# Optimization experiments

Hardware: AMD Instinct MI355X
Metric: run time of the kernel (lower is better)

Reference implementation:

```python
import jax, jax.numpy as jnp
import numpy as np

N = 50000   # num nodes
E = 800000  # num edges (avg degree 16)
D = 64      # input feature dim
H = 64      # hidden dim
O = 32      # output dim


def setup_inputs() -> dict:
    key = jax.random.key(0)
    ks = jax.random.split(key, 8)
    def lin(k, fan_in, fan_out):
        # Kaiming-uniform-ish init, stored as [in, out] so forward is x @ W
        bound = 1.0 / np.sqrt(fan_in)
        return jax.random.uniform(k, (fan_in, fan_out), jnp.float32, -bound, bound)
    return {
        "x": jax.random.normal(ks[0], (N, D), jnp.float32),
        "edge_index": jax.random.randint(ks[1], (2, E), 0, N),
        "W_in1": lin(ks[2], D, H),
        "W_neigh1": lin(ks[3], D, H),
        "bias1": jnp.zeros((H,), jnp.float32),
        "W_in2": lin(ks[4], H, H),
        "W_neigh2": lin(ks[5], H, H),
        "bias2": jnp.zeros((H,), jnp.float32),
        "W_out": lin(ks[6], H, O),
        "b_out": jnp.zeros((O,), jnp.float32),
    }


def reference(x, edge_index, W_in1, W_neigh1, bias1, W_in2, W_neigh2, bias2, W_out, b_out):
    row, col = edge_index[0], edge_index[1]  # source, target
    # get_laplacian(sym) + remove_self_loops + negate -> norm = d^-1/2[row] * d^-1/2[col]
    deg = jax.ops.segment_sum(jnp.ones((E,), x.dtype), row, num_segments=N)
    dinv = jnp.where(deg > 0, deg ** -0.5, jnp.zeros((), x.dtype))
    norm = dinv[row] * dinv[col]  # [E]

    def conv(h, W_in, W_neigh, bias):
        # message: gather transformed source features, scale by per-edge norm
        msg = (h @ W_neigh)[row] * norm[:, None]          # [E, out]
        agg = jax.ops.segment_sum(msg, col, num_segments=N)  # scatter-add -> [N, out]
        return h @ W_in + agg + bias[None, :]

    h = jax.nn.relu(conv(x, W_in1, W_neigh1, bias1))
    h = jax.nn.relu(conv(h, W_in2, W_neigh2, bias2))
    return h @ W_out + b_out[None, :]  # variant='equi': per-node output [N, O]
```

## Files before the change

### kernel.cpp

```cpp
#include <hip/hip_runtime.h>
#include <hip/hip_bf16.h>


#define NCHUNK 32
#define NRANGE_B 8
#define HIST_B2 6272
#define SMEM1 100352

typedef __attribute__((ext_vector_type(8))) short bfrag;
typedef __attribute__((ext_vector_type(4))) float f32x4;

template <bool RELU, bool PRESCALE>
__device__ __forceinline__ void gemm_tile16(
    const float* h, const float* __restrict__ dinv,
    const short* Wn_f, const short* Wi_f, const float* b_s,
    __hip_bfloat16* __restrict__ t, float* agg, int r0, int lane, int N) {
  const int m = lane & 15;
  const int quad = lane >> 4;

  bfrag Bn[4][2], Bi[4][2];
#pragma unroll
  for (int ct = 0; ct < 4; ++ct)
#pragma unroll
    for (int kb = 0; kb < 2; ++kb) {
      Bn[ct][kb] = *(const bfrag*)&Wn_f[((ct * 2 + kb) * 64 + lane) * 8];
      Bi[ct][kb] = *(const bfrag*)&Wi_f[((ct * 2 + kb) * 64 + lane) * 8];
    }

  const int arow = r0 + m;
  bfrag A[2];
#pragma unroll
  for (int kb = 0; kb < 2; ++kb) {
    bfrag av = {};
    if (arow < N) {
      const float* src = &h[(size_t)arow * 64 + kb * 32 + quad * 8];
      float4 f0 = *(const float4*)src;
      float4 f1 = *(const float4*)(src + 4);
      float tmp[8] = {f0.x, f0.y, f0.z, f0.w, f1.x, f1.y, f1.z, f1.w};
#pragma unroll
      for (int j = 0; j < 8; ++j) {
        float v = RELU ? fmaxf(tmp[j], 0.f) : tmp[j];
        __hip_bfloat16 hb = __float2bfloat16(v);
        av[j] = *(short*)&hb;
      }
    }
    A[kb] = av;
  }

  f32x4 accT[4], accA[4];
#pragma unroll
  for (int ct = 0; ct < 4; ++ct) {
    f32x4 z = {0.f, 0.f, 0.f, 0.f};
    accT[ct] = z;
    accA[ct] = z;
  }
#pragma unroll
  for (int ct = 0; ct < 4; ++ct) {
    accT[ct] = __builtin_amdgcn_mfma_f32_16x16x32_bf16(A[0], Bn[ct][0], accT[ct], 0, 0, 0);
    accT[ct] = __builtin_amdgcn_mfma_f32_16x16x32_bf16(A[1], Bn[ct][1], accT[ct], 0, 0, 0);
    accA[ct] = __builtin_amdgcn_mfma_f32_16x16x32_bf16(A[0], Bi[ct][0], accA[ct], 0, 0, 0);
    accA[ct] = __builtin_amdgcn_mfma_f32_16x16x32_bf16(A[1], Bi[ct][1], accA[ct], 0, 0, 0);
  }

#pragma unroll
  for (int reg = 0; reg < 4; ++reg) {
    int r = r0 + quad * 4 + reg;
    if (r < N) {
      float dv = PRESCALE ? dinv[r] : 1.0f;
#pragma unroll
      for (int ct = 0; ct < 4; ++ct) {
        int col = ct * 16 + m;
        float tv = PRESCALE ? accT[ct][reg] * dv : accT[ct][reg];
        t[(size_t)r * 64 + col] = __float2bfloat16(tv);
        agg[(size_t)r * 64 + col] = accA[ct][reg] + b_s[col];
      }
    }
  }
}

__device__ __forceinline__ void stage_W_frag(const float* __restrict__ Wn,
                                             const float* __restrict__ Wi,
                                             short* Wn_f, short* Wi_f,
                                             int tid, int nthr) {
  for (int i = tid; i < 4096; i += nthr) {
    int k = i >> 6, n = i & 63;
    int dst = (((n >> 4) * 2 + (k >> 5)) * 64 + ((k >> 3) & 3) * 16 + (n & 15)) * 8 + (k & 7);
    __hip_bfloat16 a = __float2bfloat16(Wn[i]);
    __hip_bfloat16 b = __float2bfloat16(Wi[i]);
    Wn_f[dst] = *(short*)&a;
    Wi_f[dst] = *(short*)&b;
  }
}

__global__ __launch_bounds__(1024) void k_hist_gemm1(
    const int* __restrict__ ei, unsigned short* __restrict__ partial,
    const float* __restrict__ x,
    const float* __restrict__ Wn, const float* __restrict__ Wi,
    const float* __restrict__ bias,
    __hip_bfloat16* __restrict__ t, float* __restrict__ agg,
    int N, int E, int gemmBlocks) {
  __shared__ __align__(16) char smem[SMEM1];
  const int tid = threadIdx.x;

  if ((int)blockIdx.x < gemmBlocks) {
    short* Wn_f = (short*)smem;
    short* Wi_f = (short*)(smem + 8192);
    float* b_s = (float*)(smem + 16384);
    stage_W_frag(Wn, Wi, Wn_f, Wi_f, tid, 1024);
    if (tid < 64) b_s[tid] = bias[tid];
    __syncthreads();
    int w = tid >> 6;
    int lane = tid & 63;
    int r0 = blockIdx.x * 256 + w * 16;
    gemm_tile16<false, false>(x, nullptr, Wn_f, Wi_f, b_s, t, agg, r0, lane, N);
    return;
  }

  int* histw = (int*)smem;
  int bid = blockIdx.x - gemmBlocks;
  int c = bid % NCHUNK;
  int a = bid / NCHUNK;
  const int* ids = ei + (size_t)a * E;
  const int sw = (N + 1) & ~1;
  const int words = sw >> 1;
  for (int i = tid; i < words; i += 1024) histw[i] = 0;
  __syncthreads();
  int e0 = (int)((long long)E * c / NCHUNK);
  int e1 = (int)((long long)E * (c + 1) / NCHUNK);
  for (int e = e0 + tid; e < e1; e += 1024) {
    int s = ids[e];
    atomicAdd(&histw[s >> 1], 1 << ((s & 1) * 16));
  }
  __syncthreads();
  int* pdst = (int*)partial + (size_t)(a * NCHUNK + c) * words;
  for (int i = tid; i < words; i += 1024) pdst[i] = histw[i];
}

__global__ __launch_bounds__(256) void k_dinv_scan(const unsigned short* __restrict__ partial,
                                                   float* __restrict__ dinv,
                                                   int* __restrict__ indeg,
                                                   int* __restrict__ ptr,
                                                   int* __restrict__ bsum, int N) {
  __shared__ int s[256];
  const int sw = (N + 1) & ~1;
  int g = blockIdx.x * 256 + threadIdx.x;
  int deg = 0, ind = 0;
  if (g < N) {
#pragma unroll
    for (int c = 0; c < NCHUNK; ++c) {
      deg += partial[(size_t)c * sw + g];
      ind += partial[(size_t)(NCHUNK + c) * sw + g];
    }
    dinv[g] = (deg > 0) ? (1.0f / sqrtf((float)deg)) : 0.0f;
    indeg[g] = ind;
  }
  s[threadIdx.x] = ind;
  __syncthreads();
  for (int off = 1; off < 256; off <<= 1) {
    int tv = (threadIdx.x >= off) ? s[threadIdx.x - off] : 0;
    __syncthreads();
    s[threadIdx.x] += tv;
    __syncthreads();
  }
  if (g < N) ptr[g] = s[threadIdx.x] - ind;
  if (threadIdx.x == 255) bsum[blockIdx.x] = s[255];
}

__global__ __launch_bounds__(256) void k_base(const unsigned short* __restrict__ partial,
                                              const int* __restrict__ bsum,
                                              int* __restrict__ ptr,
                                              int* __restrict__ base, int N, int nb) {
  __shared__ int sb[256];
  const int sw = (N + 1) & ~1;
  int v = (threadIdx.x < nb) ? bsum[threadIdx.x] : 0;
  sb[threadIdx.x] = v;
  __syncthreads();
  for (int off = 1; off < 256; off <<= 1) {
    int tv = (threadIdx.x >= off) ? sb[threadIdx.x - off] : 0;
    __syncthreads();
    sb[threadIdx.x] += tv;
    __syncthreads();
  }
  __shared__ int pbs[256];
  pbs[threadIdx.x] = sb[threadIdx.x] - v;
  __syncthreads();
  int n = blockIdx.x * 256 + threadIdx.x;
  if (n >= N) return;
  int run = ptr[n] + pbs[n >> 8];
  ptr[n] = run;
#pragma unroll
  for (int c = 0; c < NCHUNK; ++c) {
    base[(size_t)c * N + n] = run;
    run += partial[(size_t)(NCHUNK + c) * sw + n];
  }
}

__global__ __launch_bounds__(1024) void k_bin2(const int* __restrict__ ei,
                                               const int* __restrict__ base,
                                               int* __restrict__ csr_row,
                                               int N, int E, int range) {
  __shared__ int cnt[HIST_B2];
  int c = blockIdx.x % NCHUNK;
  int r = blockIdx.x / NCHUNK;
  const int* row = ei;
  const int* col = ei + E;
  int lo = r * range;
  int hi = min(N, lo + range);
  int len = hi - lo;
  const int* bslice = base + (size_t)c * N + lo;
  for (int i = threadIdx.x; i < len; i += 1024) cnt[i] = bslice[i];
  __syncthreads();
  int e0 = (int)((long long)E * c / NCHUNK);
  int e1 = (int)((long long)E * (c + 1) / NCHUNK);
  for (int e = e0 + threadIdx.x; e < e1; e += 1024) {
    int cl = col[e];
    if (cl >= lo && cl < hi) {
      int rw = row[e];
      int pos = atomicAdd(&cnt[cl - lo], 1);
      csr_row[pos] = rw;
    }
  }
}

__global__ __launch_bounds__(1024) void k_gather_gemm2(
    const int* __restrict__ csr_row, const int* __restrict__ ptr,
    const int* __restrict__ indeg, const float* __restrict__ dinv,
    const __hip_bfloat16* __restrict__ t1, float* __restrict__ agg,
    const float* __restrict__ Wn, const float* __restrict__ Wi,
    const float* __restrict__ bias,
    __hip_bfloat16* __restrict__ t2, int N) {
  __shared__ short Wn_f[4096];
  __shared__ short Wi_f[4096];
  __shared__ float b_s[64];
  __shared__ float hrows[64 * 68];

  const int tid = threadIdx.x;
  stage_W_frag(Wn, Wi, Wn_f, Wi_f, tid, 1024);
  if (tid < 64) b_s[tid] = bias[tid];

  const int w = tid >> 6;
  const int lane = tid & 63;
  const int q = lane >> 4;
  const int fl = lane & 15;
  const int nn = w * 4 + q;
  const int base = (int)blockIdx.x * 64;
  const int n = base + nn;

  if (n < N) {
    int i0 = ptr[n];
    int end = i0 + indeg[n];
    float dn = dinv[n];
    float4 acc = make_float4(0.f, 0.f, 0.f, 0.f);
    int i = i0;
    for (; i + 1 < end; i += 2) {
      int ra = csr_row[i];
      int rb = csr_row[i + 1];
      float na = dinv[ra];
      float nb = dinv[rb];
      ushort4 ua = *(const ushort4*)&t1[(size_t)ra * 64 + 4 * fl];
      ushort4 ub = *(const ushort4*)&t1[(size_t)rb * 64 + 4 * fl];
      float4 va, vb;
      ((unsigned*)&va)[0] = (unsigned)ua.x << 16; ((unsigned*)&va)[1] = (unsigned)ua.y << 16;
      ((unsigned*)&va)[2] = (unsigned)ua.z << 16; ((unsigned*)&va)[3] = (unsigned)ua.w << 16;
      ((unsigned*)&vb)[0] = (unsigned)ub.x << 16; ((unsigned*)&vb)[1] = (unsigned)ub.y << 16;
      ((unsigned*)&vb)[2] = (unsigned)ub.z << 16; ((unsigned*)&vb)[3] = (unsigned)ub.w << 16;
      acc.x = fmaf(va.x, na, acc.x); acc.y = fmaf(va.y, na, acc.y);
      acc.z = fmaf(va.z, na, acc.z); acc.w = fmaf(va.w, na, acc.w);
      acc.x = fmaf(vb.x, nb, acc.x); acc.y = fmaf(vb.y, nb, acc.y);
      acc.z = fmaf(vb.z, nb, acc.z); acc.w = fmaf(vb.w, nb, acc.w);
    }
    if (i < end) {
      int ra = csr_row[i];
      float na = dinv[ra];
      ushort4 ua = *(const ushort4*)&t1[(size_t)ra * 64 + 4 * fl];
      float4 va;
      ((unsigned*)&va)[0] = (unsigned)ua.x << 16; ((unsigned*)&va)[1] = (unsigned)ua.y << 16;
      ((unsigned*)&va)[2] = (unsigned)ua.z << 16; ((unsigned*)&va)[3] = (unsigned)ua.w << 16;
      acc.x = fmaf(va.x, na, acc.x); acc.y = fmaf(va.y, na, acc.y);
      acc.z = fmaf(va.z, na, acc.z); acc.w = fmaf(va.w, na, acc.w);
    }
    float4 aggv = *(const float4*)&agg[(size_t)n * 64 + 4 * fl];
    f32x4 hv = {aggv.x + dn * acc.x, aggv.y + dn * acc.y,
                aggv.z + dn * acc.z, aggv.w + dn * acc.w};
    *(f32x4*)&hrows[nn * 68 + 4 * fl] = hv;
  } else {
    f32x4 z = {0.f, 0.f, 0.f, 0.f};
    *(f32x4*)&hrows[nn * 68 + 4 * fl] = z;
  }
  __syncthreads();

  if (w >= 4) return;
  const int m = fl;
  const int quad = q;

  bfrag Bn[4][2], Bi[4][2];
#pragma unroll
  for (int ct = 0; ct < 4; ++ct)
#pragma unroll
    for (int kb = 0; kb < 2; ++kb) {
      Bn[ct][kb] = *(const bfrag*)&Wn_f[((ct * 2 + kb) * 64 + lane) * 8];
      Bi[ct][kb] = *(const bfrag*)&Wi_f[((ct * 2 + kb) * 64 + lane) * 8];
    }

  bfrag A[2];
#pragma unroll
  for (int kb = 0; kb < 2; ++kb) {
    const float* src = &hrows[(w * 16 + m) * 68 + kb * 32 + quad * 8];
    float4 f0 = *(const float4*)src;
    float4 f1 = *(const float4*)(src + 4);
    float tmp[8] = {f0.x, f0.y, f0.z, f0.w, f1.x, f1.y, f1.z, f1.w};
    bfrag av;
#pragma unroll
    for (int j = 0; j < 8; ++j) {
      float v = fmaxf(tmp[j], 0.f);
      __hip_bfloat16 hb = __float2bfloat16(v);
      av[j] = *(short*)&hb;
    }
    A[kb] = av;
  }

  f32x4 accT[4], accA[4];
#pragma unroll
  for (int ct = 0; ct < 4; ++ct) {
    f32x4 z = {0.f, 0.f, 0.f, 0.f};
    accT[ct] = z;
    accA[ct] = z;
  }
#pragma unroll
  for (int ct = 0; ct < 4; ++ct) {
    accT[ct] = __builtin_amdgcn_mfma_f32_16x16x32_bf16(A[0], Bn[ct][0], accT[ct], 0, 0, 0);
    accT[ct] = __builtin_amdgcn_mfma_f32_16x16x32_bf16(A[1], Bn[ct][1], accT[ct], 0, 0, 0);
    accA[ct] = __builtin_amdgcn_mfma_f32_16x16x32_bf16(A[0], Bi[ct][0], accA[ct], 0, 0, 0);
    accA[ct] = __builtin_amdgcn_mfma_f32_16x16x32_bf16(A[1], Bi[ct][1], accA[ct], 0, 0, 0);
  }

#pragma unroll
  for (int reg = 0; reg < 4; ++reg) {
    int r = base + w * 16 + quad * 4 + reg;
    if (r < N) {
      float dv = dinv[r];
#pragma unroll
      for (int ct = 0; ct < 4; ++ct) {
        int col = ct * 16 + m;
        t2[(size_t)r * 64 + col] = __float2bfloat16(accT[ct][reg] * dv);
        agg[(size_t)r * 64 + col] = accA[ct][reg] + b_s[col];
      }
    }
  }
}

__global__ __launch_bounds__(256) void k_gather_out(
    const int* __restrict__ csr_row, const int* __restrict__ ptr,
    const int* __restrict__ indeg, const float* __restrict__ dinv,
    const __hip_bfloat16* __restrict__ t, const float* __restrict__ agg,
    const float* __restrict__ Wo,
    const float* __restrict__ bo,
    float* __restrict__ out, int N) {
  __shared__ float Wo_s[64 * 32];
  __shared__ float bo_s[32];
  __shared__ float rowbuf[4][64];

  const int tid = threadIdx.x;
  for (int i = tid; i < 2048; i += 256) Wo_s[i] = Wo[i];
  if (tid < 32) bo_s[tid] = bo[tid];
  __syncthreads();

  int w = tid >> 6;
  int n = blockIdx.x * 4 + w;
  if (n >= N) return;
  int lane = tid & 63;
  int q = lane >> 4;
  int fl = lane & 15;
  int i0 = ptr[n];
  int end = i0 + indeg[n];
  float dn = dinv[n];

  float4 aggv = make_float4(0.f, 0.f, 0.f, 0.f);
  if (q == 0) aggv = *(const float4*)&agg[(size_t)n * 64 + 4 * fl];

  float4 acc = make_float4(0.f, 0.f, 0.f, 0.f);
  int i = i0 + q;
  for (; i + 4 < end; i += 8) {
    int ra = csr_row[i];
    int rb = csr_row[i + 4];
    ushort4 ua = *(const ushort4*)&t[(size_t)ra * 64 + 4 * fl];
    ushort4 ub = *(const ushort4*)&t[(size_t)rb * 64 + 4 * fl];
    float4 va, vb;
    ((unsigned*)&va)[0] = (unsigned)ua.x << 16; ((unsigned*)&va)[1] = (unsigned)ua.y << 16;
    ((unsigned*)&va)[2] = (unsigned)ua.z << 16; ((unsigned*)&va)[3] = (unsigned)ua.w << 16;
    ((unsigned*)&vb)[0] = (unsigned)ub.x << 16; ((unsigned*)&vb)[1] = (unsigned)ub.y << 16;
    ((unsigned*)&vb)[2] = (unsigned)ub.z << 16; ((unsigned*)&vb)[3] = (unsigned)ub.w << 16;
    acc.x += va.x + vb.x; acc.y += va.y + vb.y;
    acc.z += va.z + vb.z; acc.w += va.w + vb.w;
  }
  for (; i < end; i += 4) {
    int ra = csr_row[i];
    ushort4 ua = *(const ushort4*)&t[(size_t)ra * 64 + 4 * fl];
    float4 va;
    ((unsigned*)&va)[0] = (unsigned)ua.x << 16; ((unsigned*)&va)[1] = (unsigned)ua.y << 16;
    ((unsigned*)&va)[2] = (unsigned)ua.z << 16; ((unsigned*)&va)[3] = (unsigned)ua.w << 16;
    acc.x += va.x; acc.y += va.y; acc.z += va.z; acc.w += va.w;
  }
  acc.x += __shfl_xor(acc.x, 16); acc.y += __shfl_xor(acc.y, 16);
  acc.z += __shfl_xor(acc.z, 16); acc.w += __shfl_xor(acc.w, 16);
  acc.x += __shfl_xor(acc.x, 32); acc.y += __shfl_xor(acc.y, 32);
  acc.z += __shfl_xor(acc.z, 32); acc.w += __shfl_xor(acc.w, 32);
  if (q == 0) {
    rowbuf[w][4 * fl + 0] = fmaxf(aggv.x + dn * acc.x, 0.f);
    rowbuf[w][4 * fl + 1] = fmaxf(aggv.y + dn * acc.y, 0.f);
    rowbuf[w][4 * fl + 2] = fmaxf(aggv.z + dn * acc.z, 0.f);
    rowbuf[w][4 * fl + 3] = fmaxf(aggv.w + dn * acc.w, 0.f);
  }
  int half = lane >> 5;
  int j = lane & 31;
  float ov = 0.f;
#pragma unroll 8
  for (int k = 32 * half; k < 32 * half + 32; ++k)
    ov = fmaf(rowbuf[w][k], Wo_s[k * 32 + j], ov);
  ov += __shfl_xor(ov, 32);
  if (half == 0) out[(size_t)n * 32 + j] = ov + bo_s[j];
}

extern "C" void kernel_launch(void* const* d_in, const int* in_sizes, int n_in,
                              void* d_out, int out_size, void* d_ws, size_t ws_size,
                              hipStream_t stream) {
  const float* x = (const float*)d_in[0];
  const int* ei = (const int*)d_in[1];
  const float* W_in1 = (const float*)d_in[2];
  const float* W_neigh1 = (const float*)d_in[3];
  const float* bias1 = (const float*)d_in[4];
  const float* W_in2 = (const float*)d_in[5];
  const float* W_neigh2 = (const float*)d_in[6];
  const float* bias2 = (const float*)d_in[7];
  const float* W_out = (const float*)d_in[8];
  const float* b_out = (const float*)d_in[9];
  float* out = (float*)d_out;

  const int N = in_sizes[0] / 64;
  const int E = in_sizes[1] / 2;

  char* ws = (char*)d_ws;
  size_t off = 0;
  auto alloc = [&](size_t bytes) -> void* {
    void* p = ws + off;
    off += (bytes + 255) & ~(size_t)255;
    return p;
  };
  const int sw = (N + 1) & ~1;
  float* dinv = (float*)alloc((size_t)N * 4);
  int* indeg = (int*)alloc((size_t)N * 4);
  int* ptr = (int*)alloc((size_t)N * 4);
  int* bsum = (int*)alloc(1024);
  int* csr_row = (int*)alloc((size_t)E * 4);
  unsigned short* partial = (unsigned short*)alloc((size_t)2 * NCHUNK * sw * 2);
  int* base = (int*)alloc((size_t)NCHUNK * N * 4);
  __hip_bfloat16* t = (__hip_bfloat16*)alloc((size_t)N * 64 * 2);
  __hip_bfloat16* t2 = (__hip_bfloat16*)alloc((size_t)N * 64 * 2);
  float* agg = (float*)alloc((size_t)N * 64 * 4);
  (void)ws_size;

  int range_b = (N + NRANGE_B - 1) / NRANGE_B;
  int gN = (N + 255) / 256;
  int gNode = (N + 3) / 4;
  int gFused = (N + 63) / 64;
  int nb = (N + 255) / 256;
  int gemmBlocks = (N + 255) / 256;

  k_hist_gemm1<<<gemmBlocks + 2 * NCHUNK, 1024, 0, stream>>>(
      ei, partial, x, W_neigh1, W_in1, bias1, t, agg, N, E, gemmBlocks);
  k_dinv_scan<<<nb, 256, 0, stream>>>(partial, dinv, indeg, ptr, bsum, N);
  k_base<<<gN, 256, 0, stream>>>(partial, bsum, ptr, base, N, nb);
  k_bin2<<<NRANGE_B * NCHUNK, 1024, 0, stream>>>(ei, base, csr_row, N, E, range_b);

  k_gather_gemm2<<<gFused, 1024, 0, stream>>>(csr_row, ptr, indeg, dinv, t, agg,
                                              W_neigh2, W_in2, bias2, t2, N);

  k_gather_out<<<gNode, 256, 0, stream>>>(csr_row, ptr, indeg, dinv, t2, agg,
                                          W_out, b_out, out, N);
}
```

Measured before the change: 189.1 us.

## Merge degree scan and base kernels using per-range sums from histogram kernel

The histogram kernel now also computes per-256-node range totals of in-degree for each chunk and writes them to a small rsum buffer. The separate dinv/scan and base kernels are merged into one scan kernel, which scans these range totals to get block offsets directly. This removes one kernel launch and the bsum round trip between kernels. In exchange, every block redundantly scans up to 256 range sums, and the histogram blocks zero the full shared buffer and do an extra reduction pass.

```diff
diff --git a/kernel.cpp b/kernel.cpp
--- a/kernel.cpp
+++ b/kernel.cpp
@@ -98,7 +98,8 @@
     const float* __restrict__ Wn, const float* __restrict__ Wi,
     const float* __restrict__ bias,
     __hip_bfloat16* __restrict__ t, float* __restrict__ agg,
-    int N, int E, int gemmBlocks) {
+    int* __restrict__ rsum,
+    int N, int E, int gemmBlocks, int nRanges) {
   __shared__ __align__(16) char smem[SMEM1];
   const int tid = threadIdx.x;
 
@@ -123,7 +124,8 @@
   const int* ids = ei + (size_t)a * E;
   const int sw = (N + 1) & ~1;
   const int words = sw >> 1;
-  for (int i = tid; i < words; i += 1024) histw[i] = 0;
+  const int wordsPad = SMEM1 / 4;
+  for (int i = tid; i < wordsPad; i += 1024) histw[i] = 0;
   __syncthreads();
   int e0 = (int)((long long)E * c / NCHUNK);
   int e1 = (int)((long long)E * (c + 1) / NCHUNK);
@@ -134,18 +136,36 @@
   __syncthreads();
   int* pdst = (int*)partial + (size_t)(a * NCHUNK + c) * words;
   for (int i = tid; i < words; i += 1024) pdst[i] = histw[i];
-}
-
-__global__ __launch_bounds__(256) void k_dinv_scan(const unsigned short* __restrict__ partial,
-                                                   float* __restrict__ dinv,
-                                                   int* __restrict__ indeg,
-                                                   int* __restrict__ ptr,
-                                                   int* __restrict__ bsum, int N) {
+  if (a == 1) {
+    for (int i = tid; i < nRanges; i += 1024) {
+      int acc = 0;
+#pragma unroll 8
+      for (int wdx = i * 128; wdx < i * 128 + 128; ++wdx) {
+        int wv = histw[wdx];
+        acc += (wv & 0xffff) + (wv >> 16);
+      }
+      rsum[c * nRanges + i] = acc;
+    }
+  }
+}
+
+__global__ __launch_bounds__(256) void k_scan(const unsigned short* __restrict__ partial,
+                                              const int* __restrict__ rsum,
+                                              float* __restrict__ dinv,
+                                              int* __restrict__ indeg,
+                                              int* __restrict__ ptr,
+                                              int* __restrict__ base,
+                                              int N, int nRanges) {
   __shared__ int s[256];
+  __shared__ int sb[256];
   const int sw = (N + 1) & ~1;
-  int g = blockIdx.x * 256 + threadIdx.x;
-  int deg = 0, ind = 0;
+  const int tid = threadIdx.x;
+  const int j = blockIdx.x;
+  const int g = j * 256 + tid;
+
+  int ind = 0;
   if (g < N) {
+    int deg = 0;
 #pragma unroll
     for (int c = 0; c < NCHUNK; ++c) {
       deg += partial[(size_t)c * sw + g];
@@ -154,44 +174,34 @@
     dinv[g] = (deg > 0) ? (1.0f / sqrtf((float)deg)) : 0.0f;
     indeg[g] = ind;
   }
-  s[threadIdx.x] = ind;
+
+  s[tid] = ind;
+  int rt = 0;
+  if (tid < nRanges) {
+#pragma unroll
+    for (int c = 0; c < NCHUNK; ++c) rt += rsum[c * nRanges + tid];
+  }
+  sb[tid] = rt;
   __syncthreads();
   for (int off = 1; off < 256; off <<= 1) {
-    int tv = (threadIdx.x >= off) ? s[threadIdx.x - off] : 0;
+    int tv = (tid >= off) ? s[tid - off] : 0;
+    int tb = (tid >= off) ? sb[tid - off] : 0;
     __syncthreads();
-    s[threadIdx.x] += tv;
+    s[tid] += tv;
+    sb[tid] += tb;
     __syncthreads();
   }
-  if (g < N) ptr[g] = s[threadIdx.x] - ind;
-  if (threadIdx.x == 255) bsum[blockIdx.x] = s[255];
-}
-
-__global__ __launch_bounds__(256) void k_base(const unsigned short* __restrict__ partial,
-                                              const int* __restrict__ bsum,
-                                              int* __restrict__ ptr,
-                                              int* __restrict__ base, int N, int nb) {
-  __shared__ int sb[256];
-  const int sw = (N + 1) & ~1;
-  int v = (threadIdx.x < nb) ? bsum[threadIdx.x] : 0;
-  sb[threadIdx.x] = v;
-  __syncthreads();
-  for (int off = 1; off < 256; off <<= 1) {
-    int tv = (threadIdx.x >= off) ? sb[threadIdx.x - off] : 0;
-    __syncthreads();
-    sb[threadIdx.x] += tv;
-    __syncthreads();
-  }
-  __shared__ int pbs[256];
-  pbs[threadIdx.x] = sb[threadIdx.x] - v;
-  __syncthreads();
-  int n = blockIdx.x * 256 + threadIdx.x;
-  if (n >= N) return;
-  int run = ptr[n] + pbs[n >> 8];
-  ptr[n] = run;
-#pragma unroll
-  for (int c = 0; c < NCHUNK; ++c) {
-    base[(size_t)c * N + n] = run;
-    run += partial[(size_t)(NCHUNK + c) * sw + n];
+  const int ex = s[tid] - ind;
+  const int pbs = (j == 0) ? 0 : sb[j - 1];
+
+  if (g < N) {
+    int run = ex + pbs;
+    ptr[g] = run;
+#pragma unroll
+    for (int c = 0; c < NCHUNK; ++c) {
+      base[(size_t)c * N + g] = run;
+      run += partial[(size_t)(NCHUNK + c) * sw + g];
+    }
   }
 }
 
@@ -447,10 +457,11 @@
     return p;
   };
   const int sw = (N + 1) & ~1;
+  const int nRanges = (N + 255) / 256;
   float* dinv = (float*)alloc((size_t)N * 4);
   int* indeg = (int*)alloc((size_t)N * 4);
   int* ptr = (int*)alloc((size_t)N * 4);
-  int* bsum = (int*)alloc(1024);
+  int* rsum = (int*)alloc((size_t)NCHUNK * nRanges * 4);
   int* csr_row = (int*)alloc((size_t)E * 4);
   unsigned short* partial = (unsigned short*)alloc((size_t)2 * NCHUNK * sw * 2);
   int* base = (int*)alloc((size_t)NCHUNK * N * 4);
@@ -460,16 +471,17 @@
   (void)ws_size;
 
   int range_b = (N + NRANGE_B - 1) / NRANGE_B;
-  int gN = (N + 255) / 256;
   int gNode = (N + 3) / 4;
   int gFused = (N + 63) / 64;
-  int nb = (N + 255) / 256;
   int gemmBlocks = (N + 255) / 256;
 
   k_hist_gemm1<<<gemmBlocks + 2 * NCHUNK, 1024, 0, stream>>>(
-      ei, partial, x, W_neigh1, W_in1, bias1, t, agg, N, E, gemmBlocks);
-  k_dinv_scan<<<nb, 256, 0, stream>>>(partial, dinv, indeg, ptr, bsum, N);
-  k_base<<<gN, 256, 0, stream>>>(partial, bsum, ptr, base, N, nb);
+      ei, partial, x, W_neigh1, W_in1, bias1, t, agg, rsum, N, E, gemmBlocks,
+      nRanges);
+
+  k_scan<<<nRanges, 256, 0, stream>>>(partial, rsum, dinv, indeg, ptr, base,
+                                      N, nRanges);
+
   k_bin2<<<NRANGE_B * NCHUNK, 1024, 0, stream>>>(ei, base, csr_row, N, E, range_b);
 
   k_gather_gemm2<<<gFused, 1024, 0, stream>>>(csr_row, ptr, indeg, dinv, t, agg,
```

Result: no change. 189.1 us (+0.0%).
